# Optimization experiments

Measured on AMD Instinct MI355X. Metric: run time of the kernel, lower is better.

## Reference

```python
import jax, jax.numpy as jnp
import numpy as np

N_NODES = 50000
N_EDGES = 800000
FEATS = 128
HIDDEN = 64
CLASSES = 64


def graph_conv(x, edges):
    """GCN-style symmetric-normalized aggregation over an edge list (no self-loops;
    self information is supplied via the concat in the host module)."""
    src, dst = edges[0], edges[1]
    ones = jnp.ones((edges.shape[1],), dtype=x.dtype)
    deg = jax.ops.segment_sum(ones, dst, num_segments=N_NODES)
    inv_sqrt = jax.lax.rsqrt(jnp.maximum(deg, 1.0))
    coef = inv_sqrt[src] * inv_sqrt[dst]            # [E]
    msg = x[src] * coef[:, None]                     # [E, H] gather
    return jax.ops.segment_sum(msg, dst, num_segments=N_NODES)  # [N, H] scatter


def setup_inputs() -> dict:
    key = jax.random.key(0)
    ks = jax.random.split(key, 16)
    def lin(k, out_d, in_d):
        return jax.random.normal(k, (out_d, in_d), dtype=jnp.float32) / np.sqrt(in_d)
    x = jax.random.normal(ks[0], (N_NODES, FEATS), dtype=jnp.float32)
    edges = jax.random.randint(ks[1], (2, N_EDGES), 0, N_NODES, dtype=jnp.int64)
    return {
        "x": x,
        "edges": edges,
        "W1": lin(ks[2], HIDDEN, FEATS),
        "b1": jnp.zeros((HIDDEN,), dtype=jnp.float32),
        "W2": lin(ks[3], HIDDEN, 2 * HIDDEN),
        "A2a": lin(ks[4], HIDDEN, HIDDEN),
        "A2b": lin(ks[5], HIDDEN, HIDDEN),
        "W3": lin(ks[6], HIDDEN, 2 * HIDDEN),
        "A3a": lin(ks[7], HIDDEN, HIDDEN),
        "A3b": lin(ks[8], HIDDEN, HIDDEN),
        "W4": lin(ks[9], CLASSES, 2 * HIDDEN),
        "A4a": lin(ks[10], CLASSES, HIDDEN),
        "A4b": lin(ks[11], CLASSES, HIDDEN),
    }


def _block(x, edges, W, Aa, Ab):
    # relu(Linear(cat[x, conv(x)]) + att_a(x) * att_b(x))
    h = graph_conv(x, edges)
    cat = jnp.concatenate([x, h], axis=1)            # [N, 2H]
    return jax.nn.relu(cat @ W.T + (x @ Aa.T) * (x @ Ab.T))


def reference(x, edges, W1, b1, W2, A2a, A2b, W3, A3a, A3b, W4, A4a, A4b):
    x = jax.nn.relu(x @ W1.T + b1)                   # [N, H]
    x = _block(x, edges, W2, A2a, A2b)               # [N, H]
    x = _block(x, edges, W3, A3a, A3b)               # [N, H]
    x = _block(x, edges, W4, A4a, A4b)               # [N, C]
    return x
```

## Files before the change

### kernel.cpp

```cpp
#include <hip/hip_runtime.h>
#include <hip/hip_bf16.h>
#include <hip/hip_fp16.h>

#define N_NODES 50000
#define N_EDGES 800000
#define NTILES 3125
#define W_TOTAL 57344
#define WB2 192
#define CLS_UNITS 1024
#define CLS_STRIDE (128 * 256)
#define CLS_RANGE 6250
#define TB 782
#define ROWCAP 64

typedef __attribute__((ext_vector_type(8))) short bf16x8;
typedef __attribute__((ext_vector_type(4))) float f32x4;
typedef __attribute__((ext_vector_type(8))) unsigned short u16x8;

__device__ inline unsigned short f2bf(float f) {
    unsigned int x = __float_as_uint(f);
    unsigned int r = (x + 0x7FFF + ((x >> 16) & 1)) >> 16;
    return (unsigned short)r;
}
__device__ inline float2 h2f2(unsigned int u) {
    __half2 h = *(__half2*)&u;
    return make_float2(__low2float(h), __high2float(h));
}
__device__ inline unsigned int f22h2(float a, float b) {
    __half2 h = __floats2half2_rn(a, b);
    return *(unsigned int*)&h;
}

__global__ __launch_bounds__(256) void pass1_kernel(
    const float* __restrict__ x, const int* __restrict__ src, const int* __restrict__ dst,
    const float* __restrict__ W1, const float* __restrict__ b1,
    const float* W2, const float* A2a, const float* A2b,
    const float* W3, const float* A3a, const float* A3b,
    const float* W4, const float* A4a, const float* A4b,
    int* __restrict__ cnt, unsigned short* __restrict__ srcAp,
    unsigned short* __restrict__ wp, __half* __restrict__ Ht) {
    int tid = threadIdx.x;

    if (blockIdx.x < CLS_UNITS) {
        int cls = blockIdx.x & 7;
        int k = blockIdx.x >> 3;
        int lo = cls * CLS_RANGE, hi = lo + CLS_RANGE;
        for (int e = k * 256 + tid; e < N_EDGES; e += CLS_STRIDE) {
            int d = dst[e];
            if (d >= lo && d < hi) {
                int pos = atomicAdd(&cnt[d], 1);
                if (pos < ROWCAP) srcAp[(size_t)d * ROWCAP + pos] = (unsigned short)src[e];
            }
        }
        return;
    }
    if (blockIdx.x >= CLS_UNITS + TB) {
        int i = 8192 + (blockIdx.x - CLS_UNITS - TB) * 256 + tid;
        if (i >= W_TOTAL) return;
        float v;
        if (i < 16384)      v = W2[i - 8192];
        else if (i < 20480) v = A2a[i - 16384];
        else if (i < 24576) v = A2b[i - 20480];
        else if (i < 32768) v = W3[i - 24576];
        else if (i < 36864) v = A3a[i - 32768];
        else if (i < 40960) v = A3b[i - 36864];
        else if (i < 49152) v = W4[i - 40960];
        else if (i < 53248) v = A4a[i - 49152];
        else                v = A4b[i - 53248];
        wp[i] = f2bf(v);
        return;
    }

    int wave = ((blockIdx.x - CLS_UNITS) * 256 + tid) >> 6;
    if (wave >= NTILES) return;
    int lane = tid & 63;
    int r16 = lane & 15, quad = lane >> 4;
    int base = wave * 16;

    bf16x8 a[4];
    const float* xr = x + (size_t)(base + r16) * 128 + quad * 8;
#pragma unroll
    for (int kb = 0; kb < 4; kb++) {
        float4 f0 = *(const float4*)(xr + kb * 32);
        float4 f1 = *(const float4*)(xr + kb * 32 + 4);
        bf16x8 v;
        v[0] = (short)f2bf(f0.x); v[1] = (short)f2bf(f0.y);
        v[2] = (short)f2bf(f0.z); v[3] = (short)f2bf(f0.w);
        v[4] = (short)f2bf(f1.x); v[5] = (short)f2bf(f1.y);
        v[6] = (short)f2bf(f1.z); v[7] = (short)f2bf(f1.w);
        a[kb] = v;
    }

#pragma unroll
    for (int jt = 0; jt < 4; jt++) {
        f32x4 acc = {0.f, 0.f, 0.f, 0.f};
        const float* wr = W1 + (size_t)(jt * 16 + r16) * 128 + quad * 8;
#pragma unroll
        for (int kb = 0; kb < 4; kb++) {
            float4 g0 = *(const float4*)(wr + kb * 32);
            float4 g1 = *(const float4*)(wr + kb * 32 + 4);
            bf16x8 b;
            b[0] = (short)f2bf(g0.x); b[1] = (short)f2bf(g0.y);
            b[2] = (short)f2bf(g0.z); b[3] = (short)f2bf(g0.w);
            b[4] = (short)f2bf(g1.x); b[5] = (short)f2bf(g1.y);
            b[6] = (short)f2bf(g1.z); b[7] = (short)f2bf(g1.w);
            acc = __builtin_amdgcn_mfma_f32_16x16x32_bf16(a[kb], b, acc, 0, 0, 0);
        }
        int col = jt * 16 + r16;
        float bias = b1[col];
#pragma unroll
        for (int r = 0; r < 4; r++) {
            int row = base + quad * 4 + r;
            float v = fmaxf(acc[r] + bias, 0.f);
            Ht[(size_t)row * 64 + col] = __float2half(v);
        }
    }
}

__global__ __launch_bounds__(256) void scale_kernel(const int* __restrict__ cnt,
                                                    const __half* __restrict__ Ht,
                                                    __half* __restrict__ As,
                                                    float* __restrict__ isq,
                                                    float* __restrict__ sdeg) {
    int t = blockIdx.x * 256 + threadIdx.x;
    int row = t >> 4, sl = t & 15;
    if (row >= N_NODES) return;
    float dv = fmaxf((float)cnt[row], 1.0f);
    float is = rsqrtf(dv);
    if (sl == 0) {
        isq[row] = is;
        sdeg[row] = sqrtf(dv);
    }
    uint2 rv = *((const uint2*)(Ht + (size_t)row * 64) + sl);
    float2 fa = h2f2(rv.x), fb = h2f2(rv.y);
    uint2 ov;
    ov.x = f22h2(fa.x * is, fa.y * is);
    ov.y = f22h2(fb.x * is, fb.y * is);
    *((uint2*)(As + (size_t)row * 64) + sl) = ov;
}

__global__ __launch_bounds__(256) void conv_dense_k(const __half* __restrict__ hs,
                                                    const int* __restrict__ cnt,
                                                    const unsigned short* __restrict__ srcAp,
                                                    const float* __restrict__ isq,
                                                    const float* __restrict__ sdeg,
                                                    const unsigned short* __restrict__ wp,
                                                    const unsigned short* __restrict__ aap,
                                                    const unsigned short* __restrict__ abp,
                                                    __half* __restrict__ outs,
                                                    float* __restrict__ outf,
                                                    int finalLayer) {
    __shared__ unsigned short clds[64][64];
    int tid = threadIdx.x;
    int wv = tid >> 6;
    int lane = tid & 63;
    int t = blockIdx.x * 4 + wv;
    if (t >= NTILES) return;
    int base = t * 16;

    {
        int e8 = lane >> 3, fl = lane & 7;
        const unsigned int* hsp = (const unsigned int*)hs;
#pragma unroll
        for (int g = 0; g < 2; g++) {
            int lrow = g * 8 + e8;
            int row = base + lrow;
            int b = row * ROWCAP;
            int cv = min(cnt[row], ROWCAP);
            float acc[8];
#pragma unroll
            for (int k = 0; k < 8; k++) acc[k] = 0.f;
            for (int i = 0; i < cv; i += 8) {
                u16x8 sv = *(const u16x8*)(srcAp + b + i);
#pragma unroll
                for (int u = 0; u < 8; u++) {
                    int j = i + u;
                    int s = (int)sv[u];
                    uint4 raw = *(const uint4*)(hsp + (size_t)s * 32 + fl * 4);
                    unsigned int msk = (j < cv) ? 0xFFFFFFFFu : 0u;
                    float2 f0 = h2f2(raw.x & msk);
                    float2 f1 = h2f2(raw.y & msk);
                    float2 f2 = h2f2(raw.z & msk);
                    float2 f3 = h2f2(raw.w & msk);
                    acc[0] += f0.x; acc[1] += f0.y; acc[2] += f1.x; acc[3] += f1.y;
                    acc[4] += f2.x; acc[5] += f2.y; acc[6] += f3.x; acc[7] += f3.y;
                }
            }
            float sc = isq[row];
            u16x8 o;
#pragma unroll
            for (int k = 0; k < 8; k++) o[k] = f2bf(acc[k] * sc);
            *(u16x8*)(&clds[wv * 16 + lrow][fl * 8]) = o;
        }
    }

    int r16 = lane & 15, quad = lane >> 4;
    float rs = sdeg[base + r16];
    const unsigned int* hr = (const unsigned int*)(hs + (size_t)(base + r16) * 64) + quad * 4;
    uint4 raw0 = *(const uint4*)(hr);
    uint4 raw1 = *(const uint4*)(hr + 16);
    bf16x8 ha0, ha1;
    {
        float2 f;
        f = h2f2(raw0.x); ha0[0] = (short)f2bf(f.x * rs); ha0[1] = (short)f2bf(f.y * rs);
        f = h2f2(raw0.y); ha0[2] = (short)f2bf(f.x * rs); ha0[3] = (short)f2bf(f.y * rs);
        f = h2f2(raw0.z); ha0[4] = (short)f2bf(f.x * rs); ha0[5] = (short)f2bf(f.y * rs);
        f = h2f2(raw0.w); ha0[6] = (short)f2bf(f.x * rs); ha0[7] = (short)f2bf(f.y * rs);
        f = h2f2(raw1.x); ha1[0] = (short)f2bf(f.x * rs); ha1[1] = (short)f2bf(f.y * rs);
        f = h2f2(raw1.y); ha1[2] = (short)f2bf(f.x * rs); ha1[3] = (short)f2bf(f.y * rs);
        f = h2f2(raw1.z); ha1[4] = (short)f2bf(f.x * rs); ha1[5] = (short)f2bf(f.y * rs);
        f = h2f2(raw1.w); ha1[6] = (short)f2bf(f.x * rs); ha1[7] = (short)f2bf(f.y * rs);
    }
    bf16x8 ca0 = *(const bf16x8*)(&clds[wv * 16 + r16][quad * 8]);
    bf16x8 ca1 = *(const bf16x8*)(&clds[wv * 16 + r16][32 + quad * 8]);

    float isq4[4];
    if (!finalLayer) {
#pragma unroll
        for (int r = 0; r < 4; r++) isq4[r] = isq[base + quad * 4 + r];
    }

#pragma unroll
    for (int jt = 0; jt < 4; jt++) {
        const unsigned short* wr = wp + (size_t)(jt * 16 + r16) * 128 + quad * 8;
        const unsigned short* ar = aap + (size_t)(jt * 16 + r16) * 64 + quad * 8;
        const unsigned short* br = abp + (size_t)(jt * 16 + r16) * 64 + quad * 8;
        f32x4 P = {0.f, 0.f, 0.f, 0.f};
        f32x4 Q = {0.f, 0.f, 0.f, 0.f};
        f32x4 R = {0.f, 0.f, 0.f, 0.f};
        P = __builtin_amdgcn_mfma_f32_16x16x32_bf16(ha0, *(const bf16x8*)(wr), P, 0, 0, 0);
        P = __builtin_amdgcn_mfma_f32_16x16x32_bf16(ha1, *(const bf16x8*)(wr + 32), P, 0, 0, 0);
        P = __builtin_amdgcn_mfma_f32_16x16x32_bf16(ca0, *(const bf16x8*)(wr + 64), P, 0, 0, 0);
        P = __builtin_amdgcn_mfma_f32_16x16x32_bf16(ca1, *(const bf16x8*)(wr + 96), P, 0, 0, 0);
        Q = __builtin_amdgcn_mfma_f32_16x16x32_bf16(ha0, *(const bf16x8*)(ar), Q, 0, 0, 0);
        Q = __builtin_amdgcn_mfma_f32_16x16x32_bf16(ha1, *(const bf16x8*)(ar + 32), Q, 0, 0, 0);
        R = __builtin_amdgcn_mfma_f32_16x16x32_bf16(ha0, *(const bf16x8*)(br), R, 0, 0, 0);
        R = __builtin_amdgcn_mfma_f32_16x16x32_bf16(ha1, *(const bf16x8*)(br + 32), R, 0, 0, 0);
        int col = jt * 16 + r16;
#pragma unroll
        for (int r = 0; r < 4; r++) {
            int row = base + quad * 4 + r;
            float v = fmaxf(P[r] + Q[r] * R[r], 0.f);
            if (finalLayer) outf[(size_t)row * 64 + col] = v;
            else            outs[(size_t)row * 64 + col] = __float2half(v * isq4[r]);
        }
    }
}

extern "C" void kernel_launch(void* const* d_in, const int* in_sizes, int n_in,
                              void* d_out, int out_size, void* d_ws, size_t ws_size,
                              hipStream_t stream) {
    const float* x = (const float*)d_in[0];
    const int* edges = (const int*)d_in[1];
    const float* W1 = (const float*)d_in[2];
    const float* b1 = (const float*)d_in[3];
    const float* W2 = (const float*)d_in[4];
    const float* A2a = (const float*)d_in[5];
    const float* A2b = (const float*)d_in[6];
    const float* W3 = (const float*)d_in[7];
    const float* A3a = (const float*)d_in[8];
    const float* A3b = (const float*)d_in[9];
    const float* W4 = (const float*)d_in[10];
    const float* A4a = (const float*)d_in[11];
    const float* A4b = (const float*)d_in[12];
    float* out = (float*)d_out;

    const int* src = edges;
    const int* dst = edges + N_EDGES;

    char* p = (char*)d_ws;
    auto alloc = [&](size_t bytes) {
        char* r = p;
        p += (bytes + 255) & ~(size_t)255;
        return r;
    };
    int* cnt              = (int*)alloc(N_NODES * 4);
    float* isq            = (float*)alloc(N_NODES * 4);
    float* sdeg           = (float*)alloc(N_NODES * 4);
    unsigned short* srcAp = (unsigned short*)alloc((size_t)N_NODES * ROWCAP * 2);
    unsigned short* wpAll = (unsigned short*)alloc(W_TOTAL * 2);
    __half* Ht            = (__half*)alloc((size_t)N_NODES * 64 * 2);
    __half* As            = (__half*)alloc((size_t)N_NODES * 64 * 2);
    __half* Bs            = (__half*)alloc((size_t)N_NODES * 64 * 2);

    const unsigned short* W2p  = wpAll + 8192;
    const unsigned short* A2ap = wpAll + 16384;
    const unsigned short* A2bp = wpAll + 20480;
    const unsigned short* W3p  = wpAll + 24576;
    const unsigned short* A3ap = wpAll + 32768;
    const unsigned short* A3bp = wpAll + 36864;
    const unsigned short* W4p  = wpAll + 40960;
    const unsigned short* A4ap = wpAll + 49152;
    const unsigned short* A4bp = wpAll + 53248;

    hipMemsetAsync(cnt, 0, N_NODES * 4, stream);
    pass1_kernel<<<CLS_UNITS + TB + WB2, 256, 0, stream>>>(
        x, src, dst, W1, b1, W2, A2a, A2b, W3, A3a, A3b, W4, A4a, A4b,
        cnt, srcAp, wpAll, Ht);

    scale_kernel<<<(N_NODES * 16 + 255) / 256, 256, 0, stream>>>(cnt, Ht, As, isq, sdeg);

    conv_dense_k<<<TB, 256, 0, stream>>>(As, cnt, srcAp, isq, sdeg,
                                         W2p, A2ap, A2bp, Bs, nullptr, 0);
    conv_dense_k<<<TB, 256, 0, stream>>>(Bs, cnt, srcAp, isq, sdeg,
                                         W3p, A3ap, A3bp, As, nullptr, 0);
    conv_dense_k<<<TB, 256, 0, stream>>>(As, cnt, srcAp, isq, sdeg,
                                         W4p, A4ap, A4bp, nullptr, out, 1);
}
```

Baseline: 230.4 us.

## Gather neighbor features from an FP8 copy with zero-row padding

Scale and conv kernels now also write an FP8 (e4m3) copy of the normalized node features, and the neighbor gather reads 8 bytes per lane from it instead of 16 bytes of fp16. Padding slots in each adjacency row point to a zeroed sentinel row, which removes the per-edge mask, and the next index vector is prefetched. This roughly halves gather traffic on the memory-bound aggregation. The cost is FP8 quantization error in the summed messages plus an extra byte-wise store per output element, which risks accuracy tolerance.

```diff
diff --git a/kernel.cpp b/kernel.cpp
--- a/kernel.cpp
+++ b/kernel.cpp
@@ -12,9 +12,11 @@
 #define CLS_RANGE 6250
 #define TB 782
 #define ROWCAP 64
+#define ZROW N_NODES
 
 typedef __attribute__((ext_vector_type(8))) short bf16x8;
 typedef __attribute__((ext_vector_type(4))) float f32x4;
+typedef __attribute__((ext_vector_type(2))) float f32x2;
 typedef __attribute__((ext_vector_type(8))) unsigned short u16x8;
 
 __device__ inline unsigned short f2bf(float f) {
@@ -120,26 +122,38 @@
 __global__ __launch_bounds__(256) void scale_kernel(const int* __restrict__ cnt,
                                                     const __half* __restrict__ Ht,
                                                     __half* __restrict__ As,
+                                                    unsigned char* __restrict__ As8,
+                                                    unsigned short* __restrict__ srcAp,
                                                     float* __restrict__ isq,
                                                     float* __restrict__ sdeg) {
     int t = blockIdx.x * 256 + threadIdx.x;
     int row = t >> 4, sl = t & 15;
     if (row >= N_NODES) return;
-    float dv = fmaxf((float)cnt[row], 1.0f);
+    int c = cnt[row];
+    float dv = fmaxf((float)c, 1.0f);
     float is = rsqrtf(dv);
     if (sl == 0) {
         isq[row] = is;
         sdeg[row] = sqrtf(dv);
     }
+    int cv = min(c, ROWCAP);
+    int cvr = (cv + 7) & ~7;
+    if (sl < cvr - cv) srcAp[(size_t)row * ROWCAP + cv + sl] = (unsigned short)ZROW;
+
     uint2 rv = *((const uint2*)(Ht + (size_t)row * 64) + sl);
     float2 fa = h2f2(rv.x), fb = h2f2(rv.y);
+    float s0 = fa.x * is, s1 = fa.y * is, s2 = fb.x * is, s3 = fb.y * is;
     uint2 ov;
-    ov.x = f22h2(fa.x * is, fa.y * is);
-    ov.y = f22h2(fb.x * is, fb.y * is);
+    ov.x = f22h2(s0, s1);
+    ov.y = f22h2(s2, s3);
     *((uint2*)(As + (size_t)row * 64) + sl) = ov;
+    unsigned int w = __builtin_amdgcn_cvt_pk_fp8_f32(s0, s1, 0, false);
+    w = __builtin_amdgcn_cvt_pk_fp8_f32(s2, s3, w, true);
+    ((unsigned int*)As8)[(size_t)row * 16 + sl] = w;
 }
 
 __global__ __launch_bounds__(256) void conv_dense_k(const __half* __restrict__ hs,
+                                                    const unsigned char* __restrict__ hs8,
                                                     const int* __restrict__ cnt,
                                                     const unsigned short* __restrict__ srcAp,
                                                     const float* __restrict__ isq,
@@ -148,6 +162,7 @@
                                                     const unsigned short* __restrict__ aap,
                                                     const unsigned short* __restrict__ abp,
                                                     __half* __restrict__ outs,
+                                                    unsigned char* __restrict__ outs8,
                                                     float* __restrict__ outf,
                                                     int finalLayer) {
     __shared__ unsigned short clds[64][64];
@@ -160,36 +175,37 @@
 
     {
         int e8 = lane >> 3, fl = lane & 7;
-        const unsigned int* hsp = (const unsigned int*)hs;
 #pragma unroll
         for (int g = 0; g < 2; g++) {
             int lrow = g * 8 + e8;
             int row = base + lrow;
             int b = row * ROWCAP;
             int cv = min(cnt[row], ROWCAP);
-            float acc[8];
-#pragma unroll
-            for (int k = 0; k < 8; k++) acc[k] = 0.f;
-            for (int i = 0; i < cv; i += 8) {
-                u16x8 sv = *(const u16x8*)(srcAp + b + i);
-#pragma unroll
-                for (int u = 0; u < 8; u++) {
-                    int j = i + u;
-                    int s = (int)sv[u];
-                    uint4 raw = *(const uint4*)(hsp + (size_t)s * 32 + fl * 4);
-                    unsigned int msk = (j < cv) ? 0xFFFFFFFFu : 0u;
-                    float2 f0 = h2f2(raw.x & msk);
-                    float2 f1 = h2f2(raw.y & msk);
-                    float2 f2 = h2f2(raw.z & msk);
-                    float2 f3 = h2f2(raw.w & msk);
-                    acc[0] += f0.x; acc[1] += f0.y; acc[2] += f1.x; acc[3] += f1.y;
-                    acc[4] += f2.x; acc[5] += f2.y; acc[6] += f3.x; acc[7] += f3.y;
+            int cvr = (cv + 7) & ~7;
+            f32x2 acc01 = {0.f, 0.f}, acc23 = {0.f, 0.f};
+            f32x2 acc45 = {0.f, 0.f}, acc67 = {0.f, 0.f};
+            if (cvr) {
+                u16x8 sv = *(const u16x8*)(srcAp + b);
+                for (int i = 0; i < cvr; i += 8) {
+                    u16x8 svn = (i + 8 < cvr) ? *(const u16x8*)(srcAp + b + i + 8) : sv;
+#pragma unroll
+                    for (int u = 0; u < 8; u++) {
+                        int s = (int)sv[u];
+                        uint2 rv = *((const uint2*)(hs8 + (size_t)s * 64) + fl);
+                        acc01 += __builtin_amdgcn_cvt_pk_f32_fp8(rv.x, false);
+                        acc23 += __builtin_amdgcn_cvt_pk_f32_fp8(rv.x, true);
+                        acc45 += __builtin_amdgcn_cvt_pk_f32_fp8(rv.y, false);
+                        acc67 += __builtin_amdgcn_cvt_pk_f32_fp8(rv.y, true);
+                    }
+                    sv = svn;
                 }
             }
             float sc = isq[row];
             u16x8 o;
-#pragma unroll
-            for (int k = 0; k < 8; k++) o[k] = f2bf(acc[k] * sc);
+            o[0] = f2bf(acc01[0] * sc); o[1] = f2bf(acc01[1] * sc);
+            o[2] = f2bf(acc23[0] * sc); o[3] = f2bf(acc23[1] * sc);
+            o[4] = f2bf(acc45[0] * sc); o[5] = f2bf(acc45[1] * sc);
+            o[6] = f2bf(acc67[0] * sc); o[7] = f2bf(acc67[1] * sc);
             *(u16x8*)(&clds[wv * 16 + lrow][fl * 8]) = o;
         }
     }
@@ -241,8 +257,14 @@
         for (int r = 0; r < 4; r++) {
             int row = base + quad * 4 + r;
             float v = fmaxf(P[r] + Q[r] * R[r], 0.f);
-            if (finalLayer) outf[(size_t)row * 64 + col] = v;
-            else            outs[(size_t)row * 64 + col] = __float2half(v * isq4[r]);
+            if (finalLayer) {
+                outf[(size_t)row * 64 + col] = v;
+            } else {
+                float vs = v * isq4[r];
+                outs[(size_t)row * 64 + col] = __float2half(vs);
+                unsigned int pb = __builtin_amdgcn_cvt_pk_fp8_f32(vs, vs, 0, false);
+                outs8[(size_t)row * 64 + col] = (unsigned char)pb;
+            }
         }
     }
 }
@@ -282,6 +304,8 @@
     __half* Ht            = (__half*)alloc((size_t)N_NODES * 64 * 2);
     __half* As            = (__half*)alloc((size_t)N_NODES * 64 * 2);
     __half* Bs            = (__half*)alloc((size_t)N_NODES * 64 * 2);
+    unsigned char* As8    = (unsigned char*)alloc((size_t)(N_NODES + 1) * 64);
+    unsigned char* Bs8    = (unsigned char*)alloc((size_t)(N_NODES + 1) * 64);
 
     const unsigned short* W2p  = wpAll + 8192;
     const unsigned short* A2ap = wpAll + 16384;
@@ -294,16 +318,19 @@
     const unsigned short* A4bp = wpAll + 53248;
 
     hipMemsetAsync(cnt, 0, N_NODES * 4, stream);
+    hipMemsetAsync(As8 + (size_t)ZROW * 64, 0, 64, stream);
+    hipMemsetAsync(Bs8 + (size_t)ZROW * 64, 0, 64, stream);
     pass1_kernel<<<CLS_UNITS + TB + WB2, 256, 0, stream>>>(
         x, src, dst, W1, b1, W2, A2a, A2b, W3, A3a, A3b, W4, A4a, A4b,
         cnt, srcAp, wpAll, Ht);
 
-    scale_kernel<<<(N_NODES * 16 + 255) / 256, 256, 0, stream>>>(cnt, Ht, As, isq, sdeg);
-
-    conv_dense_k<<<TB, 256, 0, stream>>>(As, cnt, srcAp, isq, sdeg,
-                                         W2p, A2ap, A2bp, Bs, nullptr, 0);
-    conv_dense_k<<<TB, 256, 0, stream>>>(Bs, cnt, srcAp, isq, sdeg,
-                                         W3p, A3ap, A3bp, As, nullptr, 0);
-    conv_dense_k<<<TB, 256, 0, stream>>>(As, cnt, srcAp, isq, sdeg,
-                                         W4p, A4ap, A4bp, nullptr, out, 1);
-}
+    scale_kernel<<<(N_NODES * 16 + 255) / 256, 256, 0, stream>>>(
+        cnt, Ht, As, As8, srcAp, isq, sdeg);
+
+    conv_dense_k<<<TB, 256, 0, stream>>>(As, As8, cnt, srcAp, isq, sdeg,
+                                         W2p, A2ap, A2bp, Bs, Bs8, nullptr, 0);
+    conv_dense_k<<<TB, 256, 0, stream>>>(Bs, Bs8, cnt, srcAp, isq, sdeg,
+                                         W3p, A3ap, A3bp, As, As8, nullptr, 0);
+    conv_dense_k<<<TB, 256, 0, stream>>>(As, As8, cnt, srcAp, isq, sdeg,
+                                         W4p, A4ap, A4bp, nullptr, nullptr, out, 1);
+}
```

After: 232.0 us. Within noise of the previous version (+0.7%).
